# Performance work log

Hardware: AMD Instinct MI355X
Metric: run time of the kernel (lower is better)

Reference implementation:

```python
import jax, jax.numpy as jnp
import numpy as np

N = 50000      # nodes
E = 800000     # edges in normalized A (incl. self loops)
DIN = 128      # input_dim
DOUT = 64      # output_dim
BN_EPS = 1e-5
SLOPE = 0.01   # LeakyReLU default negative slope


def setup_inputs() -> dict:
    key = jax.random.key(0)
    ks = jax.random.split(key, 10)
    H = jax.random.normal(ks[0], (N, DIN), dtype=jnp.float32)
    rows = jax.random.randint(ks[1], (E,), 0, N, dtype=jnp.int32)
    cols = jax.random.randint(ks[2], (E,), 0, N, dtype=jnp.int32)
    # values of the symmetrically normalized adjacency (precomputed in __init__)
    vals = jax.random.uniform(ks[3], (E,), dtype=jnp.float32)
    # BatchNorm1d params/buffers (eval mode: use running stats)
    gamma = 1.0 + 0.1 * jax.random.normal(ks[4], (DIN,), dtype=jnp.float32)
    beta = 0.1 * jax.random.normal(ks[5], (DIN,), dtype=jnp.float32)
    run_mean = 0.1 * jax.random.normal(ks[6], (DIN,), dtype=jnp.float32)
    run_var = 0.5 + jax.random.uniform(ks[7], (DIN,), dtype=jnp.float32)
    # Linear(input_dim, output_dim)
    W = jax.random.normal(ks[8], (DIN, DOUT), dtype=jnp.float32) / np.sqrt(DIN)
    b = 0.01 * jax.random.normal(ks[9], (DOUT,), dtype=jnp.float32)
    return dict(H=H, rows=rows, cols=cols, vals=vals, gamma=gamma, beta=beta,
                run_mean=run_mean, run_var=run_var, W=W, b=b)


def reference(H, rows, cols, vals, gamma, beta, run_mean, run_var, W, b):
    # F.normalize: L2 row normalization with eps=1e-12
    norm = jnp.maximum(jnp.linalg.norm(H, axis=1, keepdims=True), 1e-12)
    Hn = H / norm
    # BatchNorm1d (eval: running stats); dropout is identity in eval
    scale = gamma * jax.lax.rsqrt(run_var + BN_EPS)
    Hb = (Hn - run_mean) * scale + beta
    # Linear projection [N, DIN] @ [DIN, DOUT]
    X = Hb @ W + b
    # SpMM: out[r] = sum_{e: rows[e]==r} vals[e] * X[cols[e]]
    msgs = vals[:, None] * X[cols]            # [E, DOUT] gather + scale
    out = jax.ops.segment_sum(msgs, rows, num_segments=N)
    # LeakyReLU
    return jnp.where(out >= 0, out, SLOPE * out)
```

## Files before the change

kernel.cpp:

```cpp
#include <hip/hip_runtime.h>
#include <hip/hip_fp16.h>

#define N_NODES 50000
#define E_EDGES 800000
#define DIN 128
#define DOUT 64
#define NBUK 196
#define BUKCAP 4608
#define CHUNK 2048
#define NBLKA 391
#define KXBLK 782
#define ASTRIDE 136

typedef short short8 __attribute__((ext_vector_type(8)));
typedef float f32x4 __attribute__((ext_vector_type(4)));

static __device__ __forceinline__ short f2bf(float f)
{
    union { float f; unsigned u; } x{f};
    const unsigned r = x.u + 0x7FFFu + ((x.u >> 16) & 1u);
    return (short)(r >> 16);
}

union SMemFront {
    struct { short A[64][ASTRIDE]; short B[64][ASTRIDE]; } x;
    struct {
        int lhist[NBUK]; int lstart[NBUK]; int lcur[NBUK]; int gbase[NBUK];
        int scn[256];
        unsigned lbinVC[CHUNK];
        unsigned short lbinBR[CHUNK];
    } a;
};

__global__ __launch_bounds__(256) void k_front(
    const float* __restrict__ H, const float* __restrict__ gamma,
    const float* __restrict__ beta, const float* __restrict__ mean,
    const float* __restrict__ var, const float* __restrict__ W,
    const float* __restrict__ bias, unsigned short* __restrict__ X16,
    const int* __restrict__ rows, const int* __restrict__ cols,
    const float* __restrict__ vals, int* __restrict__ gcursor,
    unsigned* __restrict__ midVC, unsigned char* __restrict__ midR)
{
    __shared__ SMemFront sm;
    const int t = threadIdx.x;

    if (blockIdx.x < NBLKA) {
        const int e0 = blockIdx.x * CHUNK;
        const int nC = min(CHUNK, E_EDGES - e0);

        if (t < NBUK) sm.a.lhist[t] = 0;
        __syncthreads();

        unsigned prVC[8];
        unsigned short prBR[8];
#pragma unroll
        for (int k = 0; k < 8; ++k) {
            const int e = e0 + k * 256 + t;
            if (e < E_EDGES) {
                const int r = rows[e];
                const unsigned hv = __half_as_ushort(__float2half(vals[e]));
                prVC[k] = (hv << 16) | (unsigned)cols[e];
                prBR[k] = (unsigned short)r;
                atomicAdd(&sm.a.lhist[r >> 8], 1);
            } else {
                prBR[k] = 0xFFFFu;
            }
        }
        __syncthreads();

        const int v = (t < NBUK) ? sm.a.lhist[t] : 0;
        sm.a.scn[t] = v;
        __syncthreads();
        for (int o = 1; o < 256; o <<= 1) {
            int u = 0;
            if (t >= o) u = sm.a.scn[t - o];
            __syncthreads();
            sm.a.scn[t] += u;
            __syncthreads();
        }
        if (t < NBUK) {
            const int ex = sm.a.scn[t] - v;
            sm.a.lstart[t] = ex;
            sm.a.lcur[t] = ex;
            sm.a.gbase[t] = t * BUKCAP + (v ? atomicAdd(&gcursor[t], v) : 0);
        }
        __syncthreads();

#pragma unroll
        for (int k = 0; k < 8; ++k) {
            if (prBR[k] != 0xFFFFu) {
                const int bk = prBR[k] >> 8;
                const int pos = atomicAdd(&sm.a.lcur[bk], 1);
                sm.a.lbinVC[pos] = prVC[k];
                sm.a.lbinBR[pos] = prBR[k];
            }
        }
        __syncthreads();

        for (int i = t; i < nC; i += 256) {
            const unsigned short br = sm.a.lbinBR[i];
            const int bk = br >> 8;
            const int g = sm.a.gbase[bk] + (i - sm.a.lstart[bk]);
            if (g < (bk + 1) * BUKCAP) {
                midVC[g] = sm.a.lbinVC[i];
                midR[g] = (unsigned char)(br & 255);
            }
        }
        return;
    }

    const int l = t & 63, wv = t >> 6;
    const int R0 = (blockIdx.x - NBLKA) * 64;

    {
        const int n = t >> 2, koff = (t & 3) * 32;
#pragma unroll
        for (int i = 0; i < 16; ++i) {
            const int k = koff + i * 2;
            const unsigned lo = (unsigned short)f2bf(W[k * DOUT + n]);
            const unsigned hi = (unsigned short)f2bf(W[(k + 1) * DOUT + n]);
            *(unsigned*)&sm.x.B[n][k] = lo | (hi << 16);
        }
    }
    {
        const int rloc = t >> 2, sub = t & 3;
        const int r = R0 + rloc;
        float4 h[8];
        if (r < N_NODES) {
            const float4* hp = (const float4*)(H + (size_t)r * DIN + sub * 32);
#pragma unroll
            for (int i = 0; i < 8; ++i) h[i] = hp[i];
        } else {
#pragma unroll
            for (int i = 0; i < 8; ++i) h[i] = make_float4(0.f, 0.f, 0.f, 0.f);
        }
        float ss = 0.f;
#pragma unroll
        for (int i = 0; i < 8; ++i)
            ss += h[i].x * h[i].x + h[i].y * h[i].y + h[i].z * h[i].z + h[i].w * h[i].w;
        ss += __shfl_xor(ss, 1, 64);
        ss += __shfl_xor(ss, 2, 64);
        const float inv = 1.0f / fmaxf(sqrtf(ss), 1e-12f);

        const float4* gp = (const float4*)(gamma + sub * 32);
        const float4* bp = (const float4*)(beta  + sub * 32);
        const float4* mp = (const float4*)(mean  + sub * 32);
        const float4* vp = (const float4*)(var   + sub * 32);
#pragma unroll
        for (int i = 0; i < 8; ++i) {
            const float4 g4 = gp[i], b4 = bp[i], m4 = mp[i], v4 = vp[i];
            const float s0 = g4.x * rsqrtf(v4.x + 1e-5f);
            const float s1 = g4.y * rsqrtf(v4.y + 1e-5f);
            const float s2 = g4.z * rsqrtf(v4.z + 1e-5f);
            const float s3 = g4.w * rsqrtf(v4.w + 1e-5f);
            const float e0 = h[i].x * inv * s0 + (b4.x - m4.x * s0);
            const float e1 = h[i].y * inv * s1 + (b4.y - m4.y * s1);
            const float e2 = h[i].z * inv * s2 + (b4.z - m4.z * s2);
            const float e3 = h[i].w * inv * s3 + (b4.w - m4.w * s3);
            const unsigned u0 = (unsigned short)f2bf(e0) | ((unsigned)(unsigned short)f2bf(e1) << 16);
            const unsigned u1 = (unsigned short)f2bf(e2) | ((unsigned)(unsigned short)f2bf(e3) << 16);
            *(uint2*)&sm.x.A[rloc][sub * 32 + i * 4] = make_uint2(u0, u1);
        }
    }

    const int ml = l & 15, q = l >> 4;
    f32x4 c0, c1, c2, c3;
    {
        const float b0 = bias[ml],      b1 = bias[16 + ml];
        const float b2 = bias[32 + ml], b3 = bias[48 + ml];
        c0 = f32x4{b0, b0, b0, b0};
        c1 = f32x4{b1, b1, b1, b1};
        c2 = f32x4{b2, b2, b2, b2};
        c3 = f32x4{b3, b3, b3, b3};
    }
    __syncthreads();

#pragma unroll
    for (int k0 = 0; k0 < 4; ++k0) {
        const short8 a  = *(const short8*)&sm.x.A[wv * 16 + ml][k0 * 32 + q * 8];
        const short8 b0 = *(const short8*)&sm.x.B[ml][k0 * 32 + q * 8];
        const short8 b1 = *(const short8*)&sm.x.B[16 + ml][k0 * 32 + q * 8];
        const short8 b2 = *(const short8*)&sm.x.B[32 + ml][k0 * 32 + q * 8];
        const short8 b3 = *(const short8*)&sm.x.B[48 + ml][k0 * 32 + q * 8];
        c0 = __builtin_amdgcn_mfma_f32_16x16x32_bf16(a, b0, c0, 0, 0, 0);
        c1 = __builtin_amdgcn_mfma_f32_16x16x32_bf16(a, b1, c1, 0, 0, 0);
        c2 = __builtin_amdgcn_mfma_f32_16x16x32_bf16(a, b2, c2, 0, 0, 0);
        c3 = __builtin_amdgcn_mfma_f32_16x16x32_bf16(a, b3, c3, 0, 0, 0);
    }

    __syncthreads();
    unsigned short* otile = (unsigned short*)&sm.x.A[0][0];
#pragma unroll
    for (int i = 0; i < 4; ++i) {
        const int r = wv * 16 + q * 4 + i;
        otile[r * 64 + ml]      = __half_as_ushort(__float2half(c0[i]));
        otile[r * 64 + 16 + ml] = __half_as_ushort(__float2half(c1[i]));
        otile[r * 64 + 32 + ml] = __half_as_ushort(__float2half(c2[i]));
        otile[r * 64 + 48 + ml] = __half_as_ushort(__float2half(c3[i]));
    }
    __syncthreads();
#pragma unroll
    for (int rep = 0; rep < 2; ++rep) {
        const int id = rep * 256 + t;
        const int row = id >> 3;
        const int off = (id & 7) * 8;
        if (R0 + row < N_NODES)
            *(uint4*)(X16 + (size_t)(R0 + row) * DOUT + off) =
                *(const uint4*)&otile[row * 64 + off];
    }
}

__global__ __launch_bounds__(512) void k_passB(
    const int* __restrict__ gcursor, const unsigned* __restrict__ midVC,
    const unsigned char* __restrict__ midR, unsigned* __restrict__ ev,
    int* __restrict__ rowS, int* __restrict__ rowE)
{
    __shared__ int lhist[256], scn[256], lcur[256];
    const int t = threadIdx.x;
    const int b = blockIdx.x;
    const int base = b * BUKCAP;
    const int total = min(gcursor[b], BUKCAP);

    if (t < 256) lhist[t] = 0;
    __syncthreads();
    for (int i = t; i < total; i += 512)
        atomicAdd(&lhist[midR[base + i]], 1);
    __syncthreads();

    const int v = (t < 256) ? lhist[t] : 0;
    if (t < 256) scn[t] = v;
    __syncthreads();
    for (int o = 1; o < 256; o <<= 1) {
        int u = 0;
        if (t < 256 && t >= o) u = scn[t - o];
        __syncthreads();
        if (t < 256) scn[t] += u;
        __syncthreads();
    }
    if (t < 256) {
        const int ex = scn[t] - v;
        lcur[t] = ex;
        const int gr = (b << 8) | t;
        if (gr < N_NODES) { rowS[gr] = base + ex; rowE[gr] = base + ex + v; }
    }
    __syncthreads();

    for (int i = t; i < total; i += 512) {
        const int lr = midR[base + i];
        const int pos = atomicAdd(&lcur[lr], 1);
        ev[base + pos] = midVC[base + i];
    }
}

__global__ __launch_bounds__(256) void k_spmm(
    const int* __restrict__ rowS, const int* __restrict__ rowE,
    const unsigned* __restrict__ ev, const unsigned short* __restrict__ X16,
    float* __restrict__ out)
{
    const int lane = threadIdx.x & 63;
    const int sub  = lane & 15;
    const int g4   = lane >> 4;
    const int row  = blockIdx.x * 4 + (threadIdx.x >> 6);
    const int s  = rowS[row];
    const int e2 = rowE[row];
    float a0 = 0.f, a1 = 0.f, a2 = 0.f, a3 = 0.f;
    int e = s + g4;
    for (; e + 4 < e2; e += 8) {
        const unsigned u0 = ev[e];
        const unsigned u1 = ev[e + 4];
        const uint2 x0 = *(const uint2*)(X16 + (u0 & 0xFFFFu) * DOUT + sub * 4);
        const uint2 x1 = *(const uint2*)(X16 + (u1 & 0xFFFFu) * DOUT + sub * 4);
        const float v0 = __half2float(__ushort_as_half((unsigned short)(u0 >> 16)));
        const float v1 = __half2float(__ushort_as_half((unsigned short)(u1 >> 16)));
        const float2 f00 = __half22float2(*(const __half2*)&x0.x);
        const float2 f01 = __half22float2(*(const __half2*)&x0.y);
        const float2 f10 = __half22float2(*(const __half2*)&x1.x);
        const float2 f11 = __half22float2(*(const __half2*)&x1.y);
        a0 = fmaf(v0, f00.x, a0); a1 = fmaf(v0, f00.y, a1);
        a2 = fmaf(v0, f01.x, a2); a3 = fmaf(v0, f01.y, a3);
        a0 = fmaf(v1, f10.x, a0); a1 = fmaf(v1, f10.y, a1);
        a2 = fmaf(v1, f11.x, a2); a3 = fmaf(v1, f11.y, a3);
    }
    for (; e < e2; e += 4) {
        const unsigned u = ev[e];
        const uint2 x = *(const uint2*)(X16 + (u & 0xFFFFu) * DOUT + sub * 4);
        const float v = __half2float(__ushort_as_half((unsigned short)(u >> 16)));
        const float2 f0 = __half22float2(*(const __half2*)&x.x);
        const float2 f1 = __half22float2(*(const __half2*)&x.y);
        a0 = fmaf(v, f0.x, a0); a1 = fmaf(v, f0.y, a1);
        a2 = fmaf(v, f1.x, a2); a3 = fmaf(v, f1.y, a3);
    }
    a0 += __shfl_xor(a0, 16, 64); a1 += __shfl_xor(a1, 16, 64);
    a2 += __shfl_xor(a2, 16, 64); a3 += __shfl_xor(a3, 16, 64);
    a0 += __shfl_xor(a0, 32, 64); a1 += __shfl_xor(a1, 32, 64);
    a2 += __shfl_xor(a2, 32, 64); a3 += __shfl_xor(a3, 32, 64);
    if (g4 == 0) {
        float4 r;
        r.x = (a0 >= 0.f) ? a0 : 0.01f * a0;
        r.y = (a1 >= 0.f) ? a1 : 0.01f * a1;
        r.z = (a2 >= 0.f) ? a2 : 0.01f * a2;
        r.w = (a3 >= 0.f) ? a3 : 0.01f * a3;
        *(float4*)(out + (size_t)row * DOUT + sub * 4) = r;
    }
}

extern "C" void kernel_launch(void* const* d_in, const int* in_sizes, int n_in,
                              void* d_out, int out_size, void* d_ws, size_t ws_size,
                              hipStream_t stream)
{
    const float* H     = (const float*)d_in[0];
    const int*   rows  = (const int*)  d_in[1];
    const int*   cols  = (const int*)  d_in[2];
    const float* vals  = (const float*)d_in[3];
    const float* gamma = (const float*)d_in[4];
    const float* beta  = (const float*)d_in[5];
    const float* mean  = (const float*)d_in[6];
    const float* var   = (const float*)d_in[7];
    const float* W     = (const float*)d_in[8];
    const float* bias  = (const float*)d_in[9];
    float* out = (float*)d_out;

    char* ws = (char*)d_ws;
    unsigned short* X16     = (unsigned short*)(ws);
    int*            gcursor = (int*)          (ws +  6400000);
    unsigned*       midVC   = (unsigned*)     (ws +  6400800);
    unsigned char*  midR    = (unsigned char*)(ws + 10013472);
    unsigned*       ev      = (unsigned*)     (ws + 10916640);
    int*            rowS    = (int*)          (ws + 14529312);
    int*            rowE    = (int*)          (ws + 14730016);

    hipMemsetAsync(gcursor, 0, NBUK * sizeof(int), stream);

    k_front<<<NBLKA + KXBLK, 256, 0, stream>>>(H, gamma, beta, mean, var, W,
                                               bias, X16, rows, cols, vals,
                                               gcursor, midVC, midR);
    k_passB<<<NBUK, 512, 0, stream>>>(gcursor, midVC, midR, ev, rowS, rowE);
    k_spmm<<<N_NODES / 4, 256, 0, stream>>>(rowS, rowE, ev, X16, out);
}
```

Before: 153.8 us.

## Fuse bucket sort and SpMM into one kernel using shared-memory edge lists

```diff
diff --git a/kernel.cpp b/kernel.cpp
--- a/kernel.cpp
+++ b/kernel.cpp
@@ -210,97 +210,104 @@
     }
 }
 
-__global__ __launch_bounds__(512) void k_passB(
+__global__ __launch_bounds__(512) void k_back(
     const int* __restrict__ gcursor, const unsigned* __restrict__ midVC,
-    const unsigned char* __restrict__ midR, unsigned* __restrict__ ev,
-    int* __restrict__ rowS, int* __restrict__ rowE)
+    const unsigned char* __restrict__ midR,
+    const unsigned short* __restrict__ X16, float* __restrict__ out)
 {
-    __shared__ int lhist[256], scn[256], lcur[256];
+    __shared__ int lhist[128], scn[128], lcur[128], lrowS[128], lrowE[128];
+    __shared__ unsigned evl[BUKCAP];
     const int t = threadIdx.x;
-    const int b = blockIdx.x;
+    const int b    = blockIdx.x >> 1;
+    const int r0   = (blockIdx.x & 1) << 7;
     const int base = b * BUKCAP;
     const int total = min(gcursor[b], BUKCAP);
 
-    if (t < 256) lhist[t] = 0;
-    __syncthreads();
-    for (int i = t; i < total; i += 512)
-        atomicAdd(&lhist[midR[base + i]], 1);
-    __syncthreads();
-
-    const int v = (t < 256) ? lhist[t] : 0;
-    if (t < 256) scn[t] = v;
-    __syncthreads();
-    for (int o = 1; o < 256; o <<= 1) {
+    if (t < 128) lhist[t] = 0;
+    __syncthreads();
+
+    for (int i = t; i < total; i += 512) {
+        const int lr = (int)midR[base + i] - r0;
+        if ((unsigned)lr < 128u) atomicAdd(&lhist[lr], 1);
+    }
+    __syncthreads();
+
+    const int v = (t < 128) ? lhist[t] : 0;
+    if (t < 128) scn[t] = v;
+    __syncthreads();
+    for (int o = 1; o < 128; o <<= 1) {
         int u = 0;
-        if (t < 256 && t >= o) u = scn[t - o];
-        __syncthreads();
-        if (t < 256) scn[t] += u;
-        __syncthreads();
-    }
-    if (t < 256) {
+        if (t < 128 && t >= o) u = scn[t - o];
+        __syncthreads();
+        if (t < 128) scn[t] += u;
+        __syncthreads();
+    }
+    if (t < 128) {
         const int ex = scn[t] - v;
         lcur[t] = ex;
-        const int gr = (b << 8) | t;
-        if (gr < N_NODES) { rowS[gr] = base + ex; rowE[gr] = base + ex + v; }
+        lrowS[t] = ex;
+        lrowE[t] = ex + v;
     }
     __syncthreads();
 
     for (int i = t; i < total; i += 512) {
-        const int lr = midR[base + i];
-        const int pos = atomicAdd(&lcur[lr], 1);
-        ev[base + pos] = midVC[base + i];
-    }
-}
-
-__global__ __launch_bounds__(256) void k_spmm(
-    const int* __restrict__ rowS, const int* __restrict__ rowE,
-    const unsigned* __restrict__ ev, const unsigned short* __restrict__ X16,
-    float* __restrict__ out)
-{
-    const int lane = threadIdx.x & 63;
+        const int lr = (int)midR[base + i] - r0;
+        if ((unsigned)lr < 128u) {
+            const int pos = atomicAdd(&lcur[lr], 1);
+            evl[pos] = midVC[base + i];
+        }
+    }
+    __syncthreads();
+
+    const int lane = t & 63;
+    const int wv   = t >> 6;
     const int sub  = lane & 15;
     const int g4   = lane >> 4;
-    const int row  = blockIdx.x * 4 + (threadIdx.x >> 6);
-    const int s  = rowS[row];
-    const int e2 = rowE[row];
-    float a0 = 0.f, a1 = 0.f, a2 = 0.f, a3 = 0.f;
-    int e = s + g4;
-    for (; e + 4 < e2; e += 8) {
-        const unsigned u0 = ev[e];
-        const unsigned u1 = ev[e + 4];
-        const uint2 x0 = *(const uint2*)(X16 + (u0 & 0xFFFFu) * DOUT + sub * 4);
-        const uint2 x1 = *(const uint2*)(X16 + (u1 & 0xFFFFu) * DOUT + sub * 4);
-        const float v0 = __half2float(__ushort_as_half((unsigned short)(u0 >> 16)));
-        const float v1 = __half2float(__ushort_as_half((unsigned short)(u1 >> 16)));
-        const float2 f00 = __half22float2(*(const __half2*)&x0.x);
-        const float2 f01 = __half22float2(*(const __half2*)&x0.y);
-        const float2 f10 = __half22float2(*(const __half2*)&x1.x);
-        const float2 f11 = __half22float2(*(const __half2*)&x1.y);
-        a0 = fmaf(v0, f00.x, a0); a1 = fmaf(v0, f00.y, a1);
-        a2 = fmaf(v0, f01.x, a2); a3 = fmaf(v0, f01.y, a3);
-        a0 = fmaf(v1, f10.x, a0); a1 = fmaf(v1, f10.y, a1);
-        a2 = fmaf(v1, f11.x, a2); a3 = fmaf(v1, f11.y, a3);
-    }
-    for (; e < e2; e += 4) {
-        const unsigned u = ev[e];
-        const uint2 x = *(const uint2*)(X16 + (u & 0xFFFFu) * DOUT + sub * 4);
-        const float v = __half2float(__ushort_as_half((unsigned short)(u >> 16)));
-        const float2 f0 = __half22float2(*(const __half2*)&x.x);
-        const float2 f1 = __half22float2(*(const __half2*)&x.y);
-        a0 = fmaf(v, f0.x, a0); a1 = fmaf(v, f0.y, a1);
-        a2 = fmaf(v, f1.x, a2); a3 = fmaf(v, f1.y, a3);
-    }
-    a0 += __shfl_xor(a0, 16, 64); a1 += __shfl_xor(a1, 16, 64);
-    a2 += __shfl_xor(a2, 16, 64); a3 += __shfl_xor(a3, 16, 64);
-    a0 += __shfl_xor(a0, 32, 64); a1 += __shfl_xor(a1, 32, 64);
-    a2 += __shfl_xor(a2, 32, 64); a3 += __shfl_xor(a3, 32, 64);
-    if (g4 == 0) {
-        float4 r;
-        r.x = (a0 >= 0.f) ? a0 : 0.01f * a0;
-        r.y = (a1 >= 0.f) ? a1 : 0.01f * a1;
-        r.z = (a2 >= 0.f) ? a2 : 0.01f * a2;
-        r.w = (a3 >= 0.f) ? a3 : 0.01f * a3;
-        *(float4*)(out + (size_t)row * DOUT + sub * 4) = r;
+#pragma unroll 1
+    for (int k = 0; k < 16; ++k) {
+        const int rr = wv * 16 + k;
+        const int grow = (b << 8) + r0 + rr;
+        const int s  = lrowS[rr];
+        const int e2 = lrowE[rr];
+        float a0 = 0.f, a1 = 0.f, a2 = 0.f, a3 = 0.f;
+        int e = s + g4;
+        for (; e + 4 < e2; e += 8) {
+            const unsigned u0 = evl[e];
+            const unsigned u1 = evl[e + 4];
+            const uint2 x0 = *(const uint2*)(X16 + (u0 & 0xFFFFu) * DOUT + sub * 4);
+            const uint2 x1 = *(const uint2*)(X16 + (u1 & 0xFFFFu) * DOUT + sub * 4);
+            const float v0 = __half2float(__ushort_as_half((unsigned short)(u0 >> 16)));
+            const float v1 = __half2float(__ushort_as_half((unsigned short)(u1 >> 16)));
+            const float2 f00 = __half22float2(*(const __half2*)&x0.x);
+            const float2 f01 = __half22float2(*(const __half2*)&x0.y);
+            const float2 f10 = __half22float2(*(const __half2*)&x1.x);
+            const float2 f11 = __half22float2(*(const __half2*)&x1.y);
+            a0 = fmaf(v0, f00.x, a0); a1 = fmaf(v0, f00.y, a1);
+            a2 = fmaf(v0, f01.x, a2); a3 = fmaf(v0, f01.y, a3);
+            a0 = fmaf(v1, f10.x, a0); a1 = fmaf(v1, f10.y, a1);
+            a2 = fmaf(v1, f11.x, a2); a3 = fmaf(v1, f11.y, a3);
+        }
+        for (; e < e2; e += 4) {
+            const unsigned u = evl[e];
+            const uint2 x = *(const uint2*)(X16 + (u & 0xFFFFu) * DOUT + sub * 4);
+            const float v2 = __half2float(__ushort_as_half((unsigned short)(u >> 16)));
+            const float2 f0 = __half22float2(*(const __half2*)&x.x);
+            const float2 f1 = __half22float2(*(const __half2*)&x.y);
+            a0 = fmaf(v2, f0.x, a0); a1 = fmaf(v2, f0.y, a1);
+            a2 = fmaf(v2, f1.x, a2); a3 = fmaf(v2, f1.y, a3);
+        }
+        a0 += __shfl_xor(a0, 16, 64); a1 += __shfl_xor(a1, 16, 64);
+        a2 += __shfl_xor(a2, 16, 64); a3 += __shfl_xor(a3, 16, 64);
+        a0 += __shfl_xor(a0, 32, 64); a1 += __shfl_xor(a1, 32, 64);
+        a2 += __shfl_xor(a2, 32, 64); a3 += __shfl_xor(a3, 32, 64);
+        if (g4 == 0 && grow < N_NODES) {
+            float4 r;
+            r.x = (a0 >= 0.f) ? a0 : 0.01f * a0;
+            r.y = (a1 >= 0.f) ? a1 : 0.01f * a1;
+            r.z = (a2 >= 0.f) ? a2 : 0.01f * a2;
+            r.w = (a3 >= 0.f) ? a3 : 0.01f * a3;
+            *(float4*)(out + (size_t)grow * DOUT + sub * 4) = r;
+        }
     }
 }
 
@@ -325,15 +332,11 @@
     int*            gcursor = (int*)          (ws +  6400000);
     unsigned*       midVC   = (unsigned*)     (ws +  6400800);
     unsigned char*  midR    = (unsigned char*)(ws + 10013472);
-    unsigned*       ev      = (unsigned*)     (ws + 10916640);
-    int*            rowS    = (int*)          (ws + 14529312);
-    int*            rowE    = (int*)          (ws + 14730016);
 
     hipMemsetAsync(gcursor, 0, NBUK * sizeof(int), stream);
 
     k_front<<<NBLKA + KXBLK, 256, 0, stream>>>(H, gamma, beta, mean, var, W,
                                                bias, X16, rows, cols, vals,
                                                gcursor, midVC, midR);
-    k_passB<<<NBUK, 512, 0, stream>>>(gcursor, midVC, midR, ev, rowS, rowE);
-    k_spmm<<<N_NODES / 4, 256, 0, stream>>>(rowS, rowE, ev, X16, out);
+    k_back<<<NBUK * 2, 512, 0, stream>>>(gcursor, midVC, midR, X16, out);
 }
```

New measurement: 152.2 us. No clear change (-1.1%).
